# Kernel optimization log

Hardware: AMD Instinct MI355X
Metric: run time of the kernel (lower is better)

Reference implementation:

```python
import jax, jax.numpy as jnp
import numpy as np

KERNEL_SIZE = 5
SIGMA = 2.0
HALF_K = KERNEL_SIZE // 2


def _gaussian_kernel():
    # torch: arange(-k//2+1, k//2+1) with python floor div -> [-2,...,2] for k=5
    ax = jnp.arange(-(KERNEL_SIZE // 2), KERNEL_SIZE // 2 + 1, dtype=jnp.float32)
    xx, yy = jnp.meshgrid(ax, ax, indexing='ij')
    k = jnp.exp(-(xx ** 2 + yy ** 2) / (2.0 * SIGMA ** 2))
    return k / k.sum()  # [5,5]


def setup_inputs() -> dict:
    key = jax.random.key(0)
    k1, k2 = jax.random.split(key)
    feature_map = jax.random.normal(k1, (512, 256, 256), dtype=jnp.float32)
    keypoints = jax.random.randint(k2, (4096, 2), 0, 256, dtype=jnp.int64)
    return {"feature_map": feature_map, "keypoints": keypoints}


def reference(feature_map, keypoints):
    C, H, W = feature_map.shape
    kern = _gaussian_kernel().astype(feature_map.dtype)  # [5,5]
    x = jnp.clip(keypoints[:, 0].astype(jnp.int32), HALF_K, W - HALF_K - 1)  # [N]
    y = jnp.clip(keypoints[:, 1].astype(jnp.int32), HALF_K, H - HALF_K - 1)  # [N]

    def pool_one(xi, yi):
        patch = jax.lax.dynamic_slice(
            feature_map, (0, yi - HALF_K, xi - HALF_K), (C, KERNEL_SIZE, KERNEL_SIZE)
        )  # [C,5,5]
        return jnp.einsum('chw,hw->c', patch, kern)  # [C]

    return jax.vmap(pool_one)(x, y)  # [N,C]
```

## Files before the change

kernel.cpp:

```cpp
#include <hip/hip_runtime.h>


#define NC  512
#define NH  256
#define NW  256
#define NKP 4096

#define OCT 8
#define SLICE_ROWS 36
#define STR 260

#define WS_LIST_OFF_I 8192

__global__ __launch_bounds__(256) void bucket_kernel(
    const int* __restrict__ kp, unsigned* __restrict__ ws_i, int n_kp)
{
    __shared__ int hist[OCT];
    __shared__ int base[OCT];
    const int t = threadIdx.x;
    const int i = blockIdx.x * 256 + t;

    if (t < OCT) hist[t] = 0;
    __syncthreads();

    int q = 0, lr = 0;
    unsigned pk = 0;
    const bool valid = (i < n_kp);
    if (valid) {
        int x = kp[2 * i + 0];
        int y = kp[2 * i + 1];
        x = min(max(x, 2), NW - 3);
        y = min(max(y, 2), NH - 3);
        q  = y >> 5;
        lr = atomicAdd(&hist[q], 1);
        pk = (unsigned)i | ((unsigned)x << 12) | ((unsigned)y << 20);
    }
    __syncthreads();

    if (t < OCT) base[t] = atomicAdd((int*)&ws_i[t], hist[t]);
    __syncthreads();

    if (valid)
        ws_i[WS_LIST_OFF_I + q * NKP + base[q] + lr] = pk;
}

__global__ __launch_bounds__(512) void pool_kernel(
    const float* __restrict__ fm, const unsigned* __restrict__ ws_i,
    float* __restrict__ out)
{
    __shared__ float plane[SLICE_ROWS * STR];

    const int c = blockIdx.x;
    const int q = blockIdx.y;
    const int t = threadIdx.x;
    const int ybase = q * 32 - 2;

    const float4* src = (const float4*)(fm + ((size_t)c << 16));
#pragma unroll
    for (int it = 0; it < 5; ++it) {
        const int i = t + it * 512;
        if (i < SLICE_ROWS * 64) {
            const int row  = i >> 6;
            const int col4 = i & 63;
            const int gr   = ybase + row;
            if ((unsigned)gr < 256u) {
                float4 v = src[(gr << 6) + col4];
                *(float4*)&plane[row * STR + (col4 << 2)] = v;
            }
        }
    }
    __syncthreads();

    const float e1 = 0.8824969025845955f;
    const float e2 = 0.6065306597126334f;
    const float s  = 2.0f * (e1 + e2) + 1.0f;
    const float inv_s2 = 1.0f / (s * s);
    const float g[5] = {e2, e1, 1.0f, e1, e2};
    float gy[5];
#pragma unroll
    for (int i = 0; i < 5; i++) gy[i] = g[i] * inv_s2;

    const int cnt = (int)ws_i[q];
    const unsigned* list = ws_i + WS_LIST_OFF_I + q * NKP;

    for (int e = t; e < cnt; e += 512) {
        const unsigned pk = list[e];
        const int n  = (int)(pk & 0xFFFu);
        const int xc = (int)((pk >> 12) & 0xFFu);
        const int yc = (int)((pk >> 20) & 0xFFu);

        const int x0 = xc - 2;
        const int r  = x0 & 3;
        const int xa = x0 - r;
        float wx[8];
#pragma unroll
        for (int i = 0; i < 8; i++)
            wx[i] = (i >= r && i < r + 5) ? g[i - r] : 0.0f;

        const int lr0 = yc - (q << 5);
        float acc = 0.0f;
#pragma unroll
        for (int dy = 0; dy < 5; dy++) {
            const float* rowp = &plane[(lr0 + dy) * STR + xa];
            float4 a = *(const float4*)rowp;
            float4 b = *(const float4*)(rowp + 4);
            acc += gy[dy] * (a.x * wx[0] + a.y * wx[1] + a.z * wx[2] + a.w * wx[3]
                           + b.x * wx[4] + b.y * wx[5] + b.z * wx[6] + b.w * wx[7]);
        }
        out[(size_t)n * NC + c] = acc;
    }
}

__global__ __launch_bounds__(256) void gpool_direct_kernel(
    const float* __restrict__ fm, const int* __restrict__ kp,
    float* __restrict__ out)
{
    const int n = blockIdx.x;
    const int t = threadIdx.x;

    int x = kp[2 * n + 0];
    int y = kp[2 * n + 1];
    x = min(max(x, 2), NW - 3);
    y = min(max(y, 2), NH - 3);

    const float e1 = 0.8824969025845955f;
    const float e2 = 0.6065306597126334f;
    const float s  = 2.0f * (e1 + e2) + 1.0f;
    const float inv_s2 = 1.0f / (s * s);
    float g[5] = {e2, e1, 1.0f, e1, e2};
    float gy[5];
#pragma unroll
    for (int i = 0; i < 5; i++) gy[i] = g[i] * inv_s2;

    const int x0 = x - 2;
    const int r  = x0 & 3;
    const int xa = x0 - r;
    float wx[8];
#pragma unroll
    for (int i = 0; i < 8; i++)
        wx[i] = (i >= r && i < r + 5) ? g[i - r] : 0.0f;

    const float* base0 = fm + ((size_t)t * NH + (y - 2)) * NW + xa;
    const float* base1 = fm + ((size_t)(t + 256) * NH + (y - 2)) * NW + xa;

    float acc0 = 0.0f, acc1 = 0.0f;
#pragma unroll
    for (int dy = 0; dy < 5; dy++) {
        const float4* p0 = (const float4*)(base0 + dy * NW);
        const float4* p1 = (const float4*)(base1 + dy * NW);
        float4 a0 = p0[0], b0 = p0[1], a1 = p1[0], b1 = p1[1];
        acc0 += gy[dy] * (a0.x * wx[0] + a0.y * wx[1] + a0.z * wx[2] + a0.w * wx[3]
                        + b0.x * wx[4] + b0.y * wx[5] + b0.z * wx[6] + b0.w * wx[7]);
        acc1 += gy[dy] * (a1.x * wx[0] + a1.y * wx[1] + a1.z * wx[2] + a1.w * wx[3]
                        + b1.x * wx[4] + b1.y * wx[5] + b1.z * wx[6] + b1.w * wx[7]);
    }

    out[(size_t)n * NC + t]       = acc0;
    out[(size_t)n * NC + t + 256] = acc1;
}

extern "C" void kernel_launch(void* const* d_in, const int* in_sizes, int n_in,
                              void* d_out, int out_size, void* d_ws, size_t ws_size,
                              hipStream_t stream)
{
    const float* fm  = (const float*)d_in[0];
    const int*   kp  = (const int*)d_in[1];
    float*       out = (float*)d_out;
    const int n_kp   = in_sizes[1] / 2;

    const size_t need = (WS_LIST_OFF_I + (size_t)OCT * NKP) * sizeof(unsigned);
    if (ws_size >= need && n_kp == NKP) {
        unsigned* ws_i = (unsigned*)d_ws;

        hipMemsetAsync(d_ws, 0, OCT * sizeof(unsigned), stream);

        bucket_kernel<<<(NKP + 255) / 256, 256, 0, stream>>>(kp, ws_i, n_kp);

        dim3 pgrid(NC, OCT);
        pool_kernel<<<pgrid, 512, 0, stream>>>(fm, ws_i, out);
    } else {
        gpool_direct_kernel<<<n_kp, 256, 0, stream>>>(fm, kp, out);
    }
}
```

Measured before the change: 210.7 us.

## Stream channel plane through LDS ring buffer with register prefetch per strip

Replaces the grid of (channel, 32-row band) blocks, each loading a 36-row halo slice, with one block per channel. That block walks 16 strips of 16 rows, keeping a 64-row ring buffer in shared memory. The next strip is prefetched into registers while keypoints of the current strip are pooled, which removes the halo re-reads and overlaps global loads with compute. In exchange each channel's work is serialised inside a single block: the grid drops to 512 blocks and there are two barriers per strip, which lowers parallelism and could reduce occupancy.

```diff
diff --git a/kernel.cpp b/kernel.cpp
--- a/kernel.cpp
+++ b/kernel.cpp
@@ -6,21 +6,20 @@
 #define NW  256
 #define NKP 4096
 
-#define OCT 8
-#define SLICE_ROWS 36
-#define STR 260
+#define NSTRIP 16
+#define RING_ROWS 64
 
 #define WS_LIST_OFF_I 8192
 
 __global__ __launch_bounds__(256) void bucket_kernel(
     const int* __restrict__ kp, unsigned* __restrict__ ws_i, int n_kp)
 {
-    __shared__ int hist[OCT];
-    __shared__ int base[OCT];
+    __shared__ int hist[NSTRIP];
+    __shared__ int base[NSTRIP];
     const int t = threadIdx.x;
     const int i = blockIdx.x * 256 + t;
 
-    if (t < OCT) hist[t] = 0;
+    if (t < NSTRIP) hist[t] = 0;
     __syncthreads();
 
     int q = 0, lr = 0;
@@ -31,83 +30,91 @@
         int y = kp[2 * i + 1];
         x = min(max(x, 2), NW - 3);
         y = min(max(y, 2), NH - 3);
-        q  = y >> 5;
+        q  = y >> 4;
         lr = atomicAdd(&hist[q], 1);
         pk = (unsigned)i | ((unsigned)x << 12) | ((unsigned)y << 20);
     }
     __syncthreads();
 
-    if (t < OCT) base[t] = atomicAdd((int*)&ws_i[t], hist[t]);
+    if (t < NSTRIP) base[t] = atomicAdd((int*)&ws_i[t], hist[t]);
     __syncthreads();
 
     if (valid)
         ws_i[WS_LIST_OFF_I + q * NKP + base[q] + lr] = pk;
 }
 
-__global__ __launch_bounds__(512) void pool_kernel(
+__global__ __launch_bounds__(256) void pool_kernel(
     const float* __restrict__ fm, const unsigned* __restrict__ ws_i,
     float* __restrict__ out)
 {
-    __shared__ float plane[SLICE_ROWS * STR];
+    __shared__ float ring[RING_ROWS * NW];
 
     const int c = blockIdx.x;
-    const int q = blockIdx.y;
     const int t = threadIdx.x;
-    const int ybase = q * 32 - 2;
-
-    const float4* src = (const float4*)(fm + ((size_t)c << 16));
-#pragma unroll
-    for (int it = 0; it < 5; ++it) {
-        const int i = t + it * 512;
-        if (i < SLICE_ROWS * 64) {
-            const int row  = i >> 6;
-            const int col4 = i & 63;
-            const int gr   = ybase + row;
-            if ((unsigned)gr < 256u) {
-                float4 v = src[(gr << 6) + col4];
-                *(float4*)&plane[row * STR + (col4 << 2)] = v;
-            }
-        }
-    }
-    __syncthreads();
+    const float* plane = fm + ((size_t)c << 16);
 
     const float e1 = 0.8824969025845955f;
     const float e2 = 0.6065306597126334f;
-    const float s  = 2.0f * (e1 + e2) + 1.0f;
-    const float inv_s2 = 1.0f / (s * s);
+    const float s2 = 2.0f * (e1 + e2) + 1.0f;
+    const float inv_s2 = 1.0f / (s2 * s2);
     const float g[5] = {e2, e1, 1.0f, e1, e2};
     float gy[5];
 #pragma unroll
     for (int i = 0; i < 5; i++) gy[i] = g[i] * inv_s2;
 
-    const int cnt = (int)ws_i[q];
-    const unsigned* list = ws_i + WS_LIST_OFF_I + q * NKP;
+    float4 pf[4];
 
-    for (int e = t; e < cnt; e += 512) {
-        const unsigned pk = list[e];
-        const int n  = (int)(pk & 0xFFFu);
-        const int xc = (int)((pk >> 12) & 0xFFu);
-        const int yc = (int)((pk >> 20) & 0xFFu);
+    for (int s = -2; s < NSTRIP; ++s) {
+        const int sp = s + 2;
 
-        const int x0 = xc - 2;
-        const int r  = x0 & 3;
-        const int xa = x0 - r;
-        float wx[8];
+        if (sp < NSTRIP) {
+            const float4* src = (const float4*)(plane + (sp << 12));
 #pragma unroll
-        for (int i = 0; i < 8; i++)
-            wx[i] = (i >= r && i < r + 5) ? g[i - r] : 0.0f;
+            for (int j = 0; j < 4; ++j)
+                pf[j] = src[t + j * 256];
+        }
 
-        const int lr0 = yc - (q << 5);
-        float acc = 0.0f;
+        if (s >= 0) {
+            const int cnt = (int)ws_i[s];
+            const unsigned* list = ws_i + WS_LIST_OFF_I + s * NKP;
+            for (int e = t; e < cnt; e += 256) {
+                const unsigned pk = list[e];
+                const int n  = (int)(pk & 0xFFFu);
+                const int xc = (int)((pk >> 12) & 0xFFu);
+                const int yc = (int)((pk >> 20) & 0xFFu);
+
+                const int x0 = xc - 2;
+                const int r  = x0 & 3;
+                const int xa = x0 - r;
+                float wx[8];
 #pragma unroll
-        for (int dy = 0; dy < 5; dy++) {
-            const float* rowp = &plane[(lr0 + dy) * STR + xa];
-            float4 a = *(const float4*)rowp;
-            float4 b = *(const float4*)(rowp + 4);
-            acc += gy[dy] * (a.x * wx[0] + a.y * wx[1] + a.z * wx[2] + a.w * wx[3]
-                           + b.x * wx[4] + b.y * wx[5] + b.z * wx[6] + b.w * wx[7]);
+                for (int i = 0; i < 8; i++)
+                    wx[i] = (i >= r && i < r + 5) ? g[i - r] : 0.0f;
+
+                float acc = 0.0f;
+#pragma unroll
+                for (int dy = 0; dy < 5; dy++) {
+                    const int gr = yc - 2 + dy;
+                    const float* rowp = &ring[((gr & (RING_ROWS - 1)) << 8) + xa];
+                    float4 a = *(const float4*)rowp;
+                    float4 b = *(const float4*)(rowp + 4);
+                    acc += gy[dy] * (a.x * wx[0] + a.y * wx[1] + a.z * wx[2] + a.w * wx[3]
+                                   + b.x * wx[4] + b.y * wx[5] + b.z * wx[6] + b.w * wx[7]);
+                }
+                out[(size_t)n * NC + c] = acc;
+            }
         }
-        out[(size_t)n * NC + c] = acc;
+
+        __syncthreads();
+
+        if (sp < NSTRIP) {
+            float* dst = &ring[(sp & 3) << 12];
+#pragma unroll
+            for (int j = 0; j < 4; ++j)
+                *(float4*)&dst[(t + j * 256) << 2] = pf[j];
+        }
+
+        __syncthreads();
     }
 }
 
@@ -168,16 +175,15 @@
     float*       out = (float*)d_out;
     const int n_kp   = in_sizes[1] / 2;
 
-    const size_t need = (WS_LIST_OFF_I + (size_t)OCT * NKP) * sizeof(unsigned);
+    const size_t need = (WS_LIST_OFF_I + (size_t)NSTRIP * NKP) * sizeof(unsigned);
     if (ws_size >= need && n_kp == NKP) {
         unsigned* ws_i = (unsigned*)d_ws;
 
-        hipMemsetAsync(d_ws, 0, OCT * sizeof(unsigned), stream);
+        hipMemsetAsync(d_ws, 0, NSTRIP * sizeof(unsigned), stream);
 
         bucket_kernel<<<(NKP + 255) / 256, 256, 0, stream>>>(kp, ws_i, n_kp);
 
-        dim3 pgrid(NC, OCT);
-        pool_kernel<<<pgrid, 512, 0, stream>>>(fm, ws_i, out);
+        pool_kernel<<<NC, 256, 0, stream>>>(fm, ws_i, out);
     } else {
         gpool_direct_kernel<<<n_kp, 256, 0, stream>>>(fm, kp, out);
     }
```

Result: slower. 227.6 us (+8.0%).

## Stage pooled results channel-major and transpose into output with a tiled kernel

Applied to the files above, without the earlier changes.

The pool kernel now writes each result into a channel-major staging buffer indexed by bucket slot, so the writes are contiguous. A new shared-memory tiled transpose kernel then scatters the staged values into the [N,C] output with coalesced row writes. This targets the strided single-float stores, 2 KB apart, that the old pool kernel issued per keypoint. The cost is an extra kernel launch, an extra read and write of the output, and a much larger workspace requirement. If the workspace is too small, the code drops to the slower direct kernel.

```diff
diff --git a/kernel.cpp b/kernel.cpp
--- a/kernel.cpp
+++ b/kernel.cpp
@@ -9,8 +9,10 @@
 #define OCT 8
 #define SLICE_ROWS 36
 #define STR 260
+#define OTS (OCT * NKP)
 
 #define WS_LIST_OFF_I 8192
+#define WS_OUTT_OFF_B (1 << 20)
 
 __global__ __launch_bounds__(256) void bucket_kernel(
     const int* __restrict__ kp, unsigned* __restrict__ ws_i, int n_kp)
@@ -46,7 +48,7 @@
 
 __global__ __launch_bounds__(512) void pool_kernel(
     const float* __restrict__ fm, const unsigned* __restrict__ ws_i,
-    float* __restrict__ out)
+    float* __restrict__ outT)
 {
     __shared__ float plane[SLICE_ROWS * STR];
 
@@ -82,10 +84,10 @@
 
     const int cnt = (int)ws_i[q];
     const unsigned* list = ws_i + WS_LIST_OFF_I + q * NKP;
+    float* orow = outT + (size_t)c * OTS + q * NKP;
 
     for (int e = t; e < cnt; e += 512) {
         const unsigned pk = list[e];
-        const int n  = (int)(pk & 0xFFFu);
         const int xc = (int)((pk >> 12) & 0xFFu);
         const int yc = (int)((pk >> 20) & 0xFFu);
 
@@ -107,7 +109,45 @@
             acc += gy[dy] * (a.x * wx[0] + a.y * wx[1] + a.z * wx[2] + a.w * wx[3]
                            + b.x * wx[4] + b.y * wx[5] + b.z * wx[6] + b.w * wx[7]);
         }
-        out[(size_t)n * NC + c] = acc;
+        orow[e] = acc;
+    }
+}
+
+__global__ __launch_bounds__(256) void outt_kernel(
+    const float* __restrict__ outT, const unsigned* __restrict__ ws_i,
+    float* __restrict__ out)
+{
+    __shared__ float tile[64][65];
+    __shared__ int n_s[64];
+    const int c0 = blockIdx.x * 64;
+    const int q  = blockIdx.y;
+    const int tx = threadIdx.x;
+    const int ty = threadIdx.y;
+
+    const int cnt = (int)ws_i[q];
+    const unsigned* list = ws_i + WS_LIST_OFF_I + q * NKP;
+
+    for (int s0 = 0; s0 < cnt; s0 += 64) {
+        const int nrem = min(64, cnt - s0);
+
+        if (ty == 0)
+            n_s[tx] = (tx < nrem) ? (int)(list[s0 + tx] & 0xFFFu) : 0;
+
+#pragma unroll
+        for (int k = 0; k < 64; k += 4) {
+            const int cc = k + ty;
+            tile[tx][cc] = (tx < nrem)
+                ? outT[(size_t)(c0 + cc) * OTS + q * NKP + s0 + tx] : 0.0f;
+        }
+        __syncthreads();
+
+#pragma unroll
+        for (int k = 0; k < 64; k += 4) {
+            const int i = k + ty;
+            if (i < nrem)
+                out[(size_t)n_s[i] * NC + c0 + tx] = tile[i][tx];
+        }
+        __syncthreads();
     }
 }
 
@@ -168,16 +208,21 @@
     float*       out = (float*)d_out;
     const int n_kp   = in_sizes[1] / 2;
 
-    const size_t need = (WS_LIST_OFF_I + (size_t)OCT * NKP) * sizeof(unsigned);
+    const size_t need = WS_OUTT_OFF_B + (size_t)NC * OTS * sizeof(float);
     if (ws_size >= need && n_kp == NKP) {
         unsigned* ws_i = (unsigned*)d_ws;
+        float* outT    = (float*)((char*)d_ws + WS_OUTT_OFF_B);
 
         hipMemsetAsync(d_ws, 0, OCT * sizeof(unsigned), stream);
 
         bucket_kernel<<<(NKP + 255) / 256, 256, 0, stream>>>(kp, ws_i, n_kp);
 
         dim3 pgrid(NC, OCT);
-        pool_kernel<<<pgrid, 512, 0, stream>>>(fm, ws_i, out);
+        pool_kernel<<<pgrid, 512, 0, stream>>>(fm, ws_i, outT);
+
+        dim3 ogrid(NC / 64, OCT);
+        dim3 oblk(64, 4);
+        outt_kernel<<<ogrid, oblk, 0, stream>>>(outT, ws_i, out);
     } else {
         gpool_direct_kernel<<<n_kp, 256, 0, stream>>>(fm, kp, out);
     }
```

Result: slower. 238.1 us (+13.0%).

## Use 16-row strips with 256-thread blocks and XCD-aware block-to-channel mapping

Applied to the files above, without the earlier changes.

Feature map rows are now split into 16 strips of 16 rows, each staged with a 2-row halo, instead of 8 strips of 32 rows. The pool kernel moves to a 1D grid of 8192 blocks with 256 threads, and the block index is decoded so that consecutive blocks land on different XCDs while strips of the same channel group share an XCD's L2. The goal is a smaller LDS footprint, more resident blocks, and better L2 locality. In exchange, halo rows are re-read more often (20 rows per 16-row strip versus 36 per 32) and the number of blocks doubles.

```diff
diff --git a/kernel.cpp b/kernel.cpp
--- a/kernel.cpp
+++ b/kernel.cpp
@@ -6,8 +6,8 @@
 #define NW  256
 #define NKP 4096
 
-#define OCT 8
-#define SLICE_ROWS 36
+#define NSTRIP 16
+#define SLICE_ROWS 20
 #define STR 260
 
 #define WS_LIST_OFF_I 8192
@@ -15,12 +15,12 @@
 __global__ __launch_bounds__(256) void bucket_kernel(
     const int* __restrict__ kp, unsigned* __restrict__ ws_i, int n_kp)
 {
-    __shared__ int hist[OCT];
-    __shared__ int base[OCT];
+    __shared__ int hist[NSTRIP];
+    __shared__ int base[NSTRIP];
     const int t = threadIdx.x;
     const int i = blockIdx.x * 256 + t;
 
-    if (t < OCT) hist[t] = 0;
+    if (t < NSTRIP) hist[t] = 0;
     __syncthreads();
 
     int q = 0, lr = 0;
@@ -31,42 +31,48 @@
         int y = kp[2 * i + 1];
         x = min(max(x, 2), NW - 3);
         y = min(max(y, 2), NH - 3);
-        q  = y >> 5;
+        q  = y >> 4;
         lr = atomicAdd(&hist[q], 1);
         pk = (unsigned)i | ((unsigned)x << 12) | ((unsigned)y << 20);
     }
     __syncthreads();
 
-    if (t < OCT) base[t] = atomicAdd((int*)&ws_i[t], hist[t]);
+    if (t < NSTRIP) base[t] = atomicAdd((int*)&ws_i[t], hist[t]);
     __syncthreads();
 
     if (valid)
         ws_i[WS_LIST_OFF_I + q * NKP + base[q] + lr] = pk;
 }
 
-__global__ __launch_bounds__(512) void pool_kernel(
+__global__ __launch_bounds__(256) void pool_kernel(
     const float* __restrict__ fm, const unsigned* __restrict__ ws_i,
     float* __restrict__ out)
 {
     __shared__ float plane[SLICE_ROWS * STR];
 
-    const int c = blockIdx.x;
-    const int q = blockIdx.y;
+    const int b     = blockIdx.x;
+    const int x7    = b & 7;
+    const int inner = b >> 3;
+    const int hi    = inner >> 8;
+    const int rem   = inner & 255;
+    const int q     = rem >> 4;
+    const int lane  = rem & 15;
+    const int chunk = (hi << 3) | x7;
+    const int c     = (chunk << 4) | lane;
+
     const int t = threadIdx.x;
-    const int ybase = q * 32 - 2;
+    const int ybase = (q << 4) - 2;
 
     const float4* src = (const float4*)(fm + ((size_t)c << 16));
 #pragma unroll
     for (int it = 0; it < 5; ++it) {
-        const int i = t + it * 512;
-        if (i < SLICE_ROWS * 64) {
-            const int row  = i >> 6;
-            const int col4 = i & 63;
-            const int gr   = ybase + row;
-            if ((unsigned)gr < 256u) {
-                float4 v = src[(gr << 6) + col4];
-                *(float4*)&plane[row * STR + (col4 << 2)] = v;
-            }
+        const int i = t + it * 256;
+        const int row  = i >> 6;
+        const int col4 = i & 63;
+        const int gr   = ybase + row;
+        if ((unsigned)gr < 256u) {
+            float4 v = src[(gr << 6) + col4];
+            *(float4*)&plane[row * STR + (col4 << 2)] = v;
         }
     }
     __syncthreads();
@@ -83,7 +89,7 @@
     const int cnt = (int)ws_i[q];
     const unsigned* list = ws_i + WS_LIST_OFF_I + q * NKP;
 
-    for (int e = t; e < cnt; e += 512) {
+    for (int e = t; e < cnt; e += 256) {
         const unsigned pk = list[e];
         const int n  = (int)(pk & 0xFFFu);
         const int xc = (int)((pk >> 12) & 0xFFu);
@@ -97,15 +103,15 @@
         for (int i = 0; i < 8; i++)
             wx[i] = (i >= r && i < r + 5) ? g[i - r] : 0.0f;
 
-        const int lr0 = yc - (q << 5);
+        const int lr0 = yc - (q << 4);
         float acc = 0.0f;
 #pragma unroll
         for (int dy = 0; dy < 5; dy++) {
             const float* rowp = &plane[(lr0 + dy) * STR + xa];
             float4 a = *(const float4*)rowp;
-            float4 b = *(const float4*)(rowp + 4);
+            float4 b4 = *(const float4*)(rowp + 4);
             acc += gy[dy] * (a.x * wx[0] + a.y * wx[1] + a.z * wx[2] + a.w * wx[3]
-                           + b.x * wx[4] + b.y * wx[5] + b.z * wx[6] + b.w * wx[7]);
+                           + b4.x * wx[4] + b4.y * wx[5] + b4.z * wx[6] + b4.w * wx[7]);
         }
         out[(size_t)n * NC + c] = acc;
     }
@@ -168,16 +174,15 @@
     float*       out = (float*)d_out;
     const int n_kp   = in_sizes[1] / 2;
 
-    const size_t need = (WS_LIST_OFF_I + (size_t)OCT * NKP) * sizeof(unsigned);
+    const size_t need = (WS_LIST_OFF_I + (size_t)NSTRIP * NKP) * sizeof(unsigned);
     if (ws_size >= need && n_kp == NKP) {
         unsigned* ws_i = (unsigned*)d_ws;
 
-        hipMemsetAsync(d_ws, 0, OCT * sizeof(unsigned), stream);
+        hipMemsetAsync(d_ws, 0, NSTRIP * sizeof(unsigned), stream);
 
         bucket_kernel<<<(NKP + 255) / 256, 256, 0, stream>>>(kp, ws_i, n_kp);
 
-        dim3 pgrid(NC, OCT);
-        pool_kernel<<<pgrid, 512, 0, stream>>>(fm, ws_i, out);
+        pool_kernel<<<NC * NSTRIP, 256, 0, stream>>>(fm, ws_i, out);
     } else {
         gpool_direct_kernel<<<n_kp, 256, 0, stream>>>(fm, kp, out);
     }
```

Measured after the change: 203.4 us. 3.5% less time.
